# Kernel tuning notes

Measured on AMD Instinct MI355X. Metric: run time of the kernel, lower is better.

## Reference

```python
import jax, jax.numpy as jnp
import numpy as np

DIM = 2048
NUM_HEADS = 16
HEAD_DIM = DIM // NUM_HEADS  # 128
B, L = 2, 2048


def setup_inputs() -> dict:
    key = jax.random.key(0)
    ks = jax.random.split(key, 5)
    x = jax.random.normal(ks[0], (B, L, DIM), dtype=jnp.float32)
    # genuine RoPE tables: inv_freq over half the head dim
    half = HEAD_DIM // 2
    inv_freq = 1.0 / (10000.0 ** (jnp.arange(half, dtype=jnp.float32) / half))
    ang = jnp.arange(L, dtype=jnp.float32)[:, None] * inv_freq[None, :]  # (L, half)
    cos = jnp.cos(ang)[:, None, :]  # (L, 1, half) broadcasts over (B,L,H,half)
    sin = jnp.sin(ang)[:, None, :]
    def dw_init(k, shape):
        fan_in, fan_out = shape
        std = 1.0 / np.sqrt(fan_in) * min(1.0, np.sqrt(fan_out / fan_in))
        return jax.random.normal(k, shape, dtype=jnp.float32) * std
    Wq = dw_init(ks[1], (DIM, DIM))
    Wk = dw_init(ks[2], (DIM, HEAD_DIM))
    Wv = dw_init(ks[3], (DIM, HEAD_DIM))
    Wo = dw_init(ks[4], (DIM, DIM))  # random instead of zeros so output is nontrivial
    return {"x": x, "cos": cos, "sin": sin, "Wq": Wq, "Wk": Wk, "Wv": Wv, "Wo": Wo}


def apply_rotary_emb(x, cos, sin):
    x1, x2 = jnp.split(x, 2, axis=-1)
    return jnp.concatenate([x1 * cos + x2 * sin, x1 * -sin + x2 * cos], axis=-1)


def rms_norm(x):
    return x * jax.lax.rsqrt(jnp.mean(x * x, axis=-1, keepdims=True) + 1e-6)


def reference(x, cos, sin, Wq, Wk, Wv, Wo):
    Bb, Ll, _ = x.shape
    q = (x @ Wq).reshape(Bb, Ll, NUM_HEADS, HEAD_DIM)  # (B,L,H,D)
    k = (x @ Wk)  # (B,L,D)  single KV head (MQA)
    v = (x @ Wv)  # (B,L,D)
    q = rms_norm(apply_rotary_emb(q, cos, sin))
    k = rms_norm(apply_rotary_emb(k[:, :, None, :], cos, sin))[:, :, 0, :]  # (B,L,D)
    scale = 1.0 / jnp.sqrt(jnp.asarray(HEAD_DIM, dtype=x.dtype))
    # scores without materializing broadcasted K: (B,H,Lq,Lk)
    scores = jnp.einsum('bqhd,bkd->bhqk', q, k) * scale
    causal = jnp.tril(jnp.ones((Ll, Ll), dtype=jnp.bool_))
    scores = jnp.where(causal[None, None], scores, jnp.asarray(-jnp.inf, dtype=scores.dtype))
    attn = jax.nn.softmax(scores, axis=-1)
    out = jnp.einsum('bhqk,bkd->bqhd', attn, v).reshape(Bb, Ll, DIM)
    return out @ Wo
```

## Files before the change

kernel.cpp:

```cpp
#include <hip/hip_runtime.h>

#define DIM 2048
#define NH 16
#define HD 128
#define BB 2
#define LL 2048
#define MROWS (BB * LL)
#define NKV 2304
#define NT 32

typedef __attribute__((ext_vector_type(8))) short short8;
typedef __attribute__((ext_vector_type(4))) float floatx4;

__device__ inline ushort f2bf(float f) {
    union { float f; unsigned u; } v; v.f = f;
    unsigned r = v.u + 0x7FFFu + ((v.u >> 16) & 1u);
    return (ushort)(r >> 16);
}

#define GL16(g, l)                                                         \
    __builtin_amdgcn_global_load_lds(                                      \
        (const __attribute__((address_space(1))) unsigned int*)(g),        \
        (__attribute__((address_space(3))) unsigned int*)(l), 16, 0, 0)

__device__ __forceinline__ short8 ld8(const ushort* p) {
    return *reinterpret_cast<const short8*>(p);
}

__global__ __launch_bounds__(256) void conv_bf16(const float* __restrict__ in,
                                                 ushort* __restrict__ out) {
    size_t i = ((size_t)blockIdx.x * 256 + threadIdx.x) * 8;
    float4 a = *reinterpret_cast<const float4*>(in + i);
    float4 b = *reinterpret_cast<const float4*>(in + i + 4);
    ushort o[8] = {f2bf(a.x), f2bf(a.y), f2bf(a.z), f2bf(a.w),
                   f2bf(b.x), f2bf(b.y), f2bf(b.z), f2bf(b.w)};
    *reinterpret_cast<uint4*>(out + i) = *reinterpret_cast<uint4*>(o);
}

__global__ __launch_bounds__(256) void wprep(const float* __restrict__ Wq,
                                             const float* __restrict__ Wk,
                                             const float* __restrict__ Wv,
                                             const float* __restrict__ Wo,
                                             ushort* __restrict__ Wcatt,
                                             ushort* __restrict__ Wot) {
    __shared__ ushort T[64][72];
    const int bid = blockIdx.x;
    const float* in;
    ushort* out;
    int in_ld, c0, r0;
    const int out_ld = 2048;
    if (bid < 1024) {
        in = Wq; out = Wcatt; in_ld = 2048;
        c0 = (bid & 31) * 64; r0 = (bid >> 5) * 64;
    } else if (bid < 2048) {
        int t = bid - 1024;
        in = Wo; out = Wot; in_ld = 2048;
        c0 = (t & 31) * 64; r0 = (t >> 5) * 64;
    } else if (bid < 2112) {
        int t = bid - 2048;
        in = Wk; out = Wcatt + (size_t)2048 * 2048; in_ld = 128;
        c0 = (t & 1) * 64; r0 = (t >> 1) * 64;
    } else {
        int t = bid - 2112;
        in = Wv; out = Wcatt + (size_t)2176 * 2048; in_ld = 128;
        c0 = (t & 1) * 64; r0 = (t >> 1) * 64;
    }
    const int tid = threadIdx.x;
#pragma unroll
    for (int rep = 0; rep < 4; ++rep) {
        int idx = tid + rep * 256;
        int r = idx >> 4, c4 = idx & 15;
        float4 f = *reinterpret_cast<const float4*>(
            in + (size_t)(r0 + r) * in_ld + c0 + c4 * 4);
        T[r][c4 * 4 + 0] = f2bf(f.x);
        T[r][c4 * 4 + 1] = f2bf(f.y);
        T[r][c4 * 4 + 2] = f2bf(f.z);
        T[r][c4 * 4 + 3] = f2bf(f.w);
    }
    __syncthreads();
#pragma unroll
    for (int rep = 0; rep < 4; ++rep) {
        int idx = tid + rep * 256;
        int cr = idx >> 4, rc4 = idx & 15;
        uint a0 = (uint)T[rc4 * 4 + 0][cr] | ((uint)T[rc4 * 4 + 1][cr] << 16);
        uint a1 = (uint)T[rc4 * 4 + 2][cr] | ((uint)T[rc4 * 4 + 3][cr] << 16);
        uint2 val = {a0, a1};
        *reinterpret_cast<uint2*>(
            out + (size_t)(c0 + cr) * out_ld + r0 + rc4 * 4) = val;
    }
}

template <int U>
__device__ __forceinline__ void stage_unit(const ushort* __restrict__ A,
                                           const ushort* __restrict__ Bt,
                                           ushort* lbase, uint offA, uint offB,
                                           int t) {
    if (t >= NT) return;
    const ushort* g = (U < 2) ? Bt : A;
    uint off = ((U < 2) ? offB : offA) + ((U & 1) ? 128u * 2048u : 0u) +
               (uint)t * 64u;
    ushort* l = lbase + U * 8192;
    GL16(g + off, l + (size_t)threadIdx.x * 8);
    GL16(g + off + 64u * 2048u, l + (size_t)(threadIdx.x + 512) * 8);
}

__global__ __launch_bounds__(512)
__attribute__((amdgpu_waves_per_eu(2, 2)))
void gemm8p(const ushort* __restrict__ A,
            const ushort* __restrict__ Bt,
            float* __restrict__ Y, int N) {
    __shared__ __attribute__((aligned(16))) ushort lds[65536];
    const int tid = threadIdx.x;
    const int lane = tid & 63;
    const int w = tid >> 6;
    const int wm = w >> 2, wn = w & 3;
    const int col = lane & 15, quad = lane >> 4;
    const int sel = col & 7;
    const int m0 = blockIdx.y * 256, n0 = blockIdx.x * 256;

    const int r0 = tid >> 3;
    const int gc0 = (tid & 7) ^ (r0 & 7);
    const uint offA = (uint)(m0 + r0) * 2048u + (uint)gc0 * 8u;
    const uint offB = (uint)(n0 + r0) * 2048u + (uint)gc0 * 8u;

    floatx4 acc[8][4];
#pragma unroll
    for (int mt = 0; mt < 8; ++mt)
#pragma unroll
        for (int nt = 0; nt < 4; ++nt) acc[mt][nt] = (floatx4){0.f, 0.f, 0.f, 0.f};

    const int aoff0 = (2 + wm) * 8192 + col * 64;
    const int boff0 = (wn >> 1) * 8192 + ((wn & 1) * 64 + col) * 64;
    const int koff0 = (quad ^ sel) * 8;
    const int koff1 = ((4 + quad) ^ sel) * 8;

    stage_unit<0>(A, Bt, lds, offA, offB, 0);
    stage_unit<1>(A, Bt, lds, offA, offB, 0);
    stage_unit<2>(A, Bt, lds, offA, offB, 0);
    stage_unit<3>(A, Bt, lds, offA, offB, 0);
    stage_unit<0>(A, Bt, lds + 32768, offA, offB, 1);
    stage_unit<1>(A, Bt, lds + 32768, offA, offB, 1);
    asm volatile("s_waitcnt vmcnt(4)" ::: "memory");
    __builtin_amdgcn_s_barrier();

#pragma unroll 2
    for (int t = 0; t < NT; ++t) {
        ushort* lb = lds + (t & 1) * 32768;
        ushort* lbn = lds + ((t + 1) & 1) * 32768;

        short8 a0[4], b0[4];
#pragma unroll
        for (int mt = 0; mt < 4; ++mt)
            a0[mt] = ld8(lb + aoff0 + mt * 1024 + koff0);
#pragma unroll
        for (int nt = 0; nt < 4; ++nt)
            b0[nt] = ld8(lb + boff0 + nt * 1024 + koff0);
        stage_unit<2>(A, Bt, lbn, offA, offB, t + 1);
        stage_unit<3>(A, Bt, lbn, offA, offB, t + 1);
        __builtin_amdgcn_s_barrier();
        asm volatile("s_waitcnt lgkmcnt(0)" ::: "memory");
        __builtin_amdgcn_s_setprio(1);
#pragma unroll
        for (int mt = 0; mt < 4; ++mt)
#pragma unroll
            for (int nt = 0; nt < 4; ++nt)
                acc[mt][nt] = __builtin_amdgcn_mfma_f32_16x16x32_bf16(
                    a0[mt], b0[nt], acc[mt][nt], 0, 0, 0);
        __builtin_amdgcn_s_setprio(0);
        __builtin_amdgcn_s_barrier();

        short8 a1[4];
#pragma unroll
        for (int mt = 0; mt < 4; ++mt)
            a1[mt] = ld8(lb + aoff0 + (4 + mt) * 1024 + koff0);
        __builtin_amdgcn_s_barrier();
        asm volatile("s_waitcnt lgkmcnt(0)" ::: "memory");
        __builtin_amdgcn_s_setprio(1);
#pragma unroll
        for (int mt = 0; mt < 4; ++mt)
#pragma unroll
            for (int nt = 0; nt < 4; ++nt)
                acc[4 + mt][nt] = __builtin_amdgcn_mfma_f32_16x16x32_bf16(
                    a1[mt], b0[nt], acc[4 + mt][nt], 0, 0, 0);
        __builtin_amdgcn_s_setprio(0);
        __builtin_amdgcn_s_barrier();

        short8 a2[4], b1[4];
#pragma unroll
        for (int mt = 0; mt < 4; ++mt)
            a2[mt] = ld8(lb + aoff0 + mt * 1024 + koff1);
#pragma unroll
        for (int nt = 0; nt < 4; ++nt)
            b1[nt] = ld8(lb + boff0 + nt * 1024 + koff1);
        __builtin_amdgcn_s_barrier();
        asm volatile("s_waitcnt lgkmcnt(0)" ::: "memory");
        __builtin_amdgcn_s_setprio(1);
#pragma unroll
        for (int mt = 0; mt < 4; ++mt)
#pragma unroll
            for (int nt = 0; nt < 4; ++nt)
                acc[mt][nt] = __builtin_amdgcn_mfma_f32_16x16x32_bf16(
                    a2[mt], b1[nt], acc[mt][nt], 0, 0, 0);
        __builtin_amdgcn_s_setprio(0);
        __builtin_amdgcn_s_barrier();

        short8 a3[4];
#pragma unroll
        for (int mt = 0; mt < 4; ++mt)
            a3[mt] = ld8(lb + aoff0 + (4 + mt) * 1024 + koff1);
        stage_unit<0>(A, Bt, lb, offA, offB, t + 2);
        stage_unit<1>(A, Bt, lb, offA, offB, t + 2);
        __builtin_amdgcn_s_barrier();
        if (t < NT - 2)
            asm volatile("s_waitcnt vmcnt(4) lgkmcnt(0)" ::: "memory");
        else
            asm volatile("s_waitcnt vmcnt(0) lgkmcnt(0)" ::: "memory");
        __builtin_amdgcn_s_setprio(1);
#pragma unroll
        for (int mt = 0; mt < 4; ++mt)
#pragma unroll
            for (int nt = 0; nt < 4; ++nt)
                acc[4 + mt][nt] = __builtin_amdgcn_mfma_f32_16x16x32_bf16(
                    a3[mt], b1[nt], acc[4 + mt][nt], 0, 0, 0);
        __builtin_amdgcn_s_setprio(0);
        __builtin_amdgcn_s_barrier();
    }

#pragma unroll
    for (int mt = 0; mt < 8; ++mt)
#pragma unroll
        for (int nt = 0; nt < 4; ++nt)
#pragma unroll
            for (int rr = 0; rr < 4; ++rr)
                Y[(size_t)(m0 + wm * 128 + mt * 16 + quad * 4 + rr) * N + n0 +
                  wn * 64 + nt * 16 + col] = acc[mt][nt][rr];
}

__global__ __launch_bounds__(256) void rope_rms_bf16(const float* __restrict__ in,
                                                     ushort* __restrict__ outb,
                                                     const float* __restrict__ cosb,
                                                     const float* __restrict__ sinb,
                                                     int heads, int nrows,
                                                     int in_ld) {
    int row = blockIdx.x * 4 + (threadIdx.x >> 6);
    int lane = threadIdx.x & 63;
    if (row >= nrows) return;
    int token = row / heads, head = row % heads;
    int l = token & (LL - 1);
    const float* p = in + (size_t)token * in_ld + head * HD;
    float x1 = p[lane];
    float x2 = p[lane + 64];
    float c = cosb[l * 64 + lane];
    float s = sinb[l * 64 + lane];
    float o1 = x1 * c + x2 * s;
    float o2 = -x1 * s + x2 * c;
    float ss = o1 * o1 + o2 * o2;
#pragma unroll
    for (int off = 32; off > 0; off >>= 1) ss += __shfl_xor(ss, off);
    float r = rsqrtf(ss * (1.0f / 128.0f) + 1e-6f);
    outb[(size_t)row * HD + lane] = f2bf(o1 * r);
    outb[(size_t)row * HD + lane + 64] = f2bf(o2 * r);
}

__global__ __launch_bounds__(256) void vtrans(const float* __restrict__ v,
                                              ushort* __restrict__ vt,
                                              int in_ld) {
    __shared__ ushort T[64][72];
    const int l0 = blockIdx.x * 64, d0 = blockIdx.y * 64, b = blockIdx.z;
    const int tid = threadIdx.x;
#pragma unroll
    for (int rep = 0; rep < 4; ++rep) {
        int idx = tid + rep * 256;
        int r = idx >> 4, c4 = idx & 15;
        float4 f = *reinterpret_cast<const float4*>(
            v + (size_t)(b * LL + l0 + r) * in_ld + d0 + c4 * 4);
        T[r][c4 * 4 + 0] = f2bf(f.x);
        T[r][c4 * 4 + 1] = f2bf(f.y);
        T[r][c4 * 4 + 2] = f2bf(f.z);
        T[r][c4 * 4 + 3] = f2bf(f.w);
    }
    __syncthreads();
#pragma unroll
    for (int rep = 0; rep < 4; ++rep) {
        int idx = tid + rep * 256;
        int dr = idx >> 4, lc4 = idx & 15;
        uint a0 = (uint)T[lc4 * 4 + 0][dr] | ((uint)T[lc4 * 4 + 1][dr] << 16);
        uint a1 = (uint)T[lc4 * 4 + 2][dr] | ((uint)T[lc4 * 4 + 3][dr] << 16);
        uint2 val = {a0, a1};
        *reinterpret_cast<uint2*>(
            vt + (size_t)(b * HD + d0 + dr) * LL + l0 + lc4 * 4) = val;
    }
}

__global__ __launch_bounds__(256) void flash_mfma(const ushort* __restrict__ qb,
                                                  const ushort* __restrict__ kb,
                                                  const ushort* __restrict__ vt,
                                                  ushort* __restrict__ aob) {
    __shared__ ushort Ks[64 * 128];
    __shared__ ushort VTs[128 * 64];
    __shared__ ushort Ps[4][16][72];

    const int tid = threadIdx.x;
    const int w = tid >> 6, lane = tid & 63;
    const int col = lane & 15, quad = lane >> 4;
    const int pairIdx = blockIdx.x, bh = blockIdx.y;
    const int b = bh >> 4, h = bh & 15;
    const int sel = col & 7;
    const float scl2 = 0.08838834764831845f * 1.44269504088896340736f;
    const float M2 = 11.5f * 1.44269504088896340736f;

    const int ksr[4] = {(tid + 0) >> 4, (tid + 256) >> 4, (tid + 512) >> 4,
                        (tid + 768) >> 4};
    const int vsr[4] = {(tid + 0) >> 3, (tid + 256) >> 3, (tid + 512) >> 3,
                        (tid + 768) >> 3};

    for (int sp = 0; sp < 2; ++sp) {
        const int qt = sp ? (31 - pairIdx) : pairIdx;
        const int q0 = qt * 64;

        const ushort* qrow =
            qb + ((size_t)(b * LL + q0 + w * 16 + col) * NH + h) * HD;
        short8 aq[4];
#pragma unroll
        for (int kc = 0; kc < 4; ++kc)
            aq[kc] = *reinterpret_cast<const short8*>(qrow + kc * 32 + quad * 8);

        float lrow[4] = {0.f, 0.f, 0.f, 0.f};
        floatx4 oacc[8];
#pragma unroll
        for (int dt = 0; dt < 8; ++dt) oacc[dt] = (floatx4){0.f, 0.f, 0.f, 0.f};

        const int ntiles = qt + 1;
        for (int kt = 0; kt < ntiles; ++kt) {
            const int k0 = kt * 64;
            __syncthreads();
#pragma unroll
            for (int rep = 0; rep < 4; ++rep) {
                int slot = tid + rep * 256;
                int r = ksr[rep];
                int gc = (slot & 15) ^ (r & 7);
                GL16(kb + (size_t)(b * LL + k0 + r) * HD + gc * 8,
                     Ks + (size_t)slot * 8);
            }
#pragma unroll
            for (int rep = 0; rep < 4; ++rep) {
                int slot = tid + rep * 256;
                int r = vsr[rep];
                int gc = (slot & 7) ^ (r & 7);
                GL16(vt + (size_t)(b * HD + r) * LL + k0 + gc * 8,
                     VTs + (size_t)slot * 8);
            }
            __syncthreads();

            floatx4 sacc[4];
#pragma unroll
            for (int nt = 0; nt < 4; ++nt)
                sacc[nt] = (floatx4){0.f, 0.f, 0.f, 0.f};
            __builtin_amdgcn_s_setprio(1);
#pragma unroll
            for (int nt = 0; nt < 4; ++nt) {
#pragma unroll
                for (int kc = 0; kc < 4; ++kc) {
                    short8 bk = *reinterpret_cast<const short8*>(
                        &Ks[(nt * 16 + col) * 128 +
                            ((kc * 4 + quad) ^ sel) * 8]);
                    sacc[nt] = __builtin_amdgcn_mfma_f32_16x16x32_bf16(
                        aq[kc], bk, sacc[nt], 0, 0, 0);
                }
            }
            __builtin_amdgcn_s_setprio(0);

            float psum[4] = {0.f, 0.f, 0.f, 0.f};
#pragma unroll
            for (int nt = 0; nt < 4; ++nt) {
                int kj = k0 + nt * 16 + col;
#pragma unroll
                for (int rr = 0; rr < 4; ++rr) {
                    int qi = q0 + w * 16 + quad * 4 + rr;
                    float p = exp2f(fmaf(sacc[nt][rr], scl2, -M2));
                    p = (kj <= qi) ? p : 0.0f;
                    sacc[nt][rr] = p;
                    psum[rr] += p;
                }
            }
#pragma unroll
            for (int rr = 0; rr < 4; ++rr) lrow[rr] += psum[rr];

#pragma unroll
            for (int nt = 0; nt < 4; ++nt)
#pragma unroll
                for (int rr = 0; rr < 4; ++rr)
                    Ps[w][quad * 4 + rr][nt * 16 + col] = f2bf(sacc[nt][rr]);
            asm volatile("s_waitcnt lgkmcnt(0)" ::: "memory");

#pragma unroll
            for (int kt2 = 0; kt2 < 2; ++kt2) {
                short8 ap = *reinterpret_cast<const short8*>(
                    &Ps[w][col][kt2 * 32 + quad * 8]);
                __builtin_amdgcn_s_setprio(1);
#pragma unroll
                for (int dt = 0; dt < 8; ++dt) {
                    short8 bv = *reinterpret_cast<const short8*>(
                        &VTs[(dt * 16 + col) * 64 +
                             ((kt2 * 4 + quad) ^ sel) * 8]);
                    oacc[dt] = __builtin_amdgcn_mfma_f32_16x16x32_bf16(
                        ap, bv, oacc[dt], 0, 0, 0);
                }
                __builtin_amdgcn_s_setprio(0);
            }
        }

#pragma unroll
        for (int off = 1; off < 16; off <<= 1)
#pragma unroll
            for (int rr = 0; rr < 4; ++rr)
                lrow[rr] += __shfl_xor(lrow[rr], off);
        float inv[4];
#pragma unroll
        for (int rr = 0; rr < 4; ++rr) inv[rr] = 1.0f / lrow[rr];
#pragma unroll
        for (int dt = 0; dt < 8; ++dt)
#pragma unroll
            for (int rr = 0; rr < 4; ++rr)
                aob[((size_t)(b * LL + q0 + w * 16 + quad * 4 + rr) * NH + h) *
                        HD + dt * 16 + col] = f2bf(oacc[dt][rr] * inv[rr]);
    }
}

extern "C" void kernel_launch(void* const* d_in, const int* in_sizes, int n_in,
                              void* d_out, int out_size, void* d_ws,
                              size_t ws_size, hipStream_t stream) {
    const float* x    = (const float*)d_in[0];
    const float* cosb = (const float*)d_in[1];
    const float* sinb = (const float*)d_in[2];
    const float* Wq   = (const float*)d_in[3];
    const float* Wk   = (const float*)d_in[4];
    const float* Wv   = (const float*)d_in[5];
    const float* Wo   = (const float*)d_in[6];
    float* out = (float*)d_out;

    float* qkv  = (float*)d_ws;
    ushort* xb  = (ushort*)(qkv + (size_t)MROWS * NKV);
    ushort* qb  = xb + (size_t)MROWS * DIM;
    ushort* kb  = qb + (size_t)MROWS * DIM;
    ushort* vt  = kb + (size_t)MROWS * HD;
    ushort* aob = vt + (size_t)MROWS * HD;
    ushort* Wcatt = aob + (size_t)MROWS * DIM;
    ushort* Wot   = Wcatt + (size_t)NKV * DIM;

    conv_bf16<<<dim3(MROWS * DIM / (256 * 8)), 256, 0, stream>>>(x, xb);
    wprep<<<dim3(2176), 256, 0, stream>>>(Wq, Wk, Wv, Wo, Wcatt, Wot);

    gemm8p<<<dim3(NKV / 256, MROWS / 256), 512, 0, stream>>>(xb, Wcatt, qkv,
                                                             NKV);

    rope_rms_bf16<<<dim3(MROWS * NH / 4), 256, 0, stream>>>(
        qkv, qb, cosb, sinb, NH, MROWS * NH, NKV);
    rope_rms_bf16<<<dim3(MROWS / 4), 256, 0, stream>>>(
        qkv + DIM, kb, cosb, sinb, 1, MROWS, NKV);
    vtrans<<<dim3(LL / 64, 2, BB), 256, 0, stream>>>(qkv + DIM + HD, vt, NKV);

    flash_mfma<<<dim3(LL / 128, BB * NH), 256, 0, stream>>>(qb, kb, vt, aob);

    gemm8p<<<dim3(DIM / 256, MROWS / 256), 512, 0, stream>>>(aob, Wot, out,
                                                             DIM);
}
```

Measured before the change: 321.2 us.

## Double-buffer K/V tiles in flash attention to overlap loads with MFMA

Splits the K and V^T shared-memory tiles into two buffers and prefetches the next key tile with async global-to-LDS loads while the current tile is processed. A partial vmcnt wait plus raw barriers replace the full __syncthreads pairs around each tile load. This hides global load latency behind the QK and PV matrix work, at the cost of doubling LDS use (lower occupancy) and relying on hand-placed waitcnt/barrier ordering.

```diff
diff --git a/kernel.cpp b/kernel.cpp
--- a/kernel.cpp
+++ b/kernel.cpp
@@ -296,8 +296,8 @@
                                                   const ushort* __restrict__ kb,
                                                   const ushort* __restrict__ vt,
                                                   ushort* __restrict__ aob) {
-    __shared__ ushort Ks[64 * 128];
-    __shared__ ushort VTs[128 * 64];
+    __shared__ ushort Ks[2][64 * 128];
+    __shared__ ushort VTs[2][128 * 64];
     __shared__ ushort Ps[4][16][72];
 
     const int tid = threadIdx.x;
@@ -309,10 +309,25 @@
     const float scl2 = 0.08838834764831845f * 1.44269504088896340736f;
     const float M2 = 11.5f * 1.44269504088896340736f;
 
-    const int ksr[4] = {(tid + 0) >> 4, (tid + 256) >> 4, (tid + 512) >> 4,
-                        (tid + 768) >> 4};
-    const int vsr[4] = {(tid + 0) >> 3, (tid + 256) >> 3, (tid + 512) >> 3,
-                        (tid + 768) >> 3};
+    auto stageKV = [&](int kt, int bf) {
+        const int k0 = kt * 64;
+#pragma unroll
+        for (int rep = 0; rep < 4; ++rep) {
+            int slot = tid + rep * 256;
+            int r = slot >> 4;
+            int gc = (slot & 15) ^ (r & 7);
+            GL16(kb + (size_t)(b * LL + k0 + r) * HD + gc * 8,
+                 &Ks[bf][0] + (size_t)slot * 8);
+        }
+#pragma unroll
+        for (int rep = 0; rep < 4; ++rep) {
+            int slot = tid + rep * 256;
+            int r = slot >> 3;
+            int gc = (slot & 7) ^ (r & 7);
+            GL16(vt + (size_t)(b * HD + r) * LL + k0 + gc * 8,
+                 &VTs[bf][0] + (size_t)slot * 8);
+        }
+    };
 
     for (int sp = 0; sp < 2; ++sp) {
         const int qt = sp ? (31 - pairIdx) : pairIdx;
@@ -330,27 +345,18 @@
 #pragma unroll
         for (int dt = 0; dt < 8; ++dt) oacc[dt] = (floatx4){0.f, 0.f, 0.f, 0.f};
 
-        const int ntiles = qt + 1;
-        for (int kt = 0; kt < ntiles; ++kt) {
+        stageKV(0, 0);
+        int cur = 0;
+
+        for (int kt = 0; kt <= qt; ++kt) {
             const int k0 = kt * 64;
-            __syncthreads();
-#pragma unroll
-            for (int rep = 0; rep < 4; ++rep) {
-                int slot = tid + rep * 256;
-                int r = ksr[rep];
-                int gc = (slot & 15) ^ (r & 7);
-                GL16(kb + (size_t)(b * LL + k0 + r) * HD + gc * 8,
-                     Ks + (size_t)slot * 8);
+            if (kt < qt) {
+                stageKV(kt + 1, cur ^ 1);
+                asm volatile("s_waitcnt vmcnt(8)" ::: "memory");
+            } else {
+                asm volatile("s_waitcnt vmcnt(0)" ::: "memory");
             }
-#pragma unroll
-            for (int rep = 0; rep < 4; ++rep) {
-                int slot = tid + rep * 256;
-                int r = vsr[rep];
-                int gc = (slot & 7) ^ (r & 7);
-                GL16(vt + (size_t)(b * HD + r) * LL + k0 + gc * 8,
-                     VTs + (size_t)slot * 8);
-            }
-            __syncthreads();
+            __builtin_amdgcn_s_barrier();
 
             floatx4 sacc[4];
 #pragma unroll
@@ -362,8 +368,8 @@
 #pragma unroll
                 for (int kc = 0; kc < 4; ++kc) {
                     short8 bk = *reinterpret_cast<const short8*>(
-                        &Ks[(nt * 16 + col) * 128 +
-                            ((kc * 4 + quad) ^ sel) * 8]);
+                        &Ks[cur][(nt * 16 + col) * 128 +
+                                 ((kc * 4 + quad) ^ sel) * 8]);
                     sacc[nt] = __builtin_amdgcn_mfma_f32_16x16x32_bf16(
                         aq[kc], bk, sacc[nt], 0, 0, 0);
                 }
@@ -401,13 +407,16 @@
 #pragma unroll
                 for (int dt = 0; dt < 8; ++dt) {
                     short8 bv = *reinterpret_cast<const short8*>(
-                        &VTs[(dt * 16 + col) * 64 +
-                             ((kt2 * 4 + quad) ^ sel) * 8]);
+                        &VTs[cur][(dt * 16 + col) * 64 +
+                                  ((kt2 * 4 + quad) ^ sel) * 8]);
                     oacc[dt] = __builtin_amdgcn_mfma_f32_16x16x32_bf16(
                         ap, bv, oacc[dt], 0, 0, 0);
                 }
                 __builtin_amdgcn_s_setprio(0);
             }
+
+            __builtin_amdgcn_s_barrier();
+            cur ^= 1;
         }
 
 #pragma unroll
```

Measured after the change: 320.2 us. No clear change (-0.3%).
